# Performance work log

Hardware: AMD Instinct MI355X
Metric: run time of the kernel (lower is better)

## Reference

```python
import jax, jax.numpy as jnp
import numpy as np

B, S, C, D, P = 32, 720, 2048, 256, 96
LATENT_DIMS = [512, 128, 32]  # enc_in // 4 ** k, e_layers=3
NL = 3
ALPHA = 0.1
EPS = 1e-5


def _ln(x, g, b, eps=1e-5):
    m = jnp.mean(x, axis=-1, keepdims=True)
    v = jnp.var(x, axis=-1, keepdims=True)
    return (x - m) * jax.lax.rsqrt(v + eps) * g + b


def _cov_loss(skips, lam=ALPHA, eps=EPS):
    total = jnp.zeros((), dtype=jnp.float32)
    for x in skips[1:]:
        b, c, d = x.shape
        xr = x.reshape(b * c, d)
        xc = (xr - jnp.mean(xr, axis=0, keepdims=True)) / (jnp.std(xr, axis=0, ddof=1, keepdims=True) + eps)
        cov = xc.T @ xc / (b * c - 1) + eps * jnp.eye(d, dtype=x.dtype)
        total = total - jnp.linalg.slogdet(cov)[1] / d
    return lam * total / (len(skips) - 1)


def setup_inputs() -> dict:
    key = jax.random.key(0)
    ks = jax.random.split(key, 16)
    w = lambda k, shp: (jax.random.normal(k, shp, dtype=jnp.float32) * 0.02)
    inp = {
        'x_enc': jax.random.normal(ks[0], (B, S, C), dtype=jnp.float32),
        'x_mark_enc': jnp.zeros((B, S, 4), dtype=jnp.float32),
        'x_dec': jnp.zeros((B, P, C), dtype=jnp.float32),
        'x_mark_dec': jnp.zeros((B, P, 4), dtype=jnp.float32),
        'in_w': w(ks[1], (S, D)), 'in_b': jnp.zeros((D,), jnp.float32),
        'lq0': jax.random.normal(ks[2], (LATENT_DIMS[0], D), dtype=jnp.float32),
        'lq1': jax.random.normal(ks[3], (LATENT_DIMS[1], D), dtype=jnp.float32),
        'lq2': jax.random.normal(ks[4], (LATENT_DIMS[2], D), dtype=jnp.float32),
        'down_w': w(ks[5], (NL, 4, D, D)), 'down_b': jnp.zeros((NL, 4, D), jnp.float32),
        'down_ln': jnp.stack([jnp.ones((NL, D)), jnp.zeros((NL, D))], axis=1).astype(jnp.float32),
        'pred_w': w(ks[6], (D, D)), 'pred_b': jnp.zeros((D,), jnp.float32),
        'up_w': w(ks[7], (NL, 4, D, D)), 'up_b': jnp.zeros((NL, 4, D), jnp.float32),
        'up_ln': jnp.stack([jnp.ones((NL, D)), jnp.zeros((NL, D))], axis=1).astype(jnp.float32),
        'out_w': w(ks[8], (D, P)), 'out_b': jnp.zeros((P,), jnp.float32),
    }
    return inp


def _forward(x_enc, in_w, in_b, lqs, down_w, down_b, down_ln,
             pred_w, pred_b, up_w, up_b, up_ln, out_w, out_b):
    # instance norm over time
    means = jnp.mean(x_enc, axis=1, keepdims=True)            # [B,1,C]
    xc = x_enc - means
    stdev = jnp.sqrt(jnp.var(xc, axis=1, keepdims=True) + 1e-5)
    xn = xc / stdev
    # transpose + Linear(seq_len -> d_model): [B,C,D]
    h = jnp.einsum('bsc,sd->bcd', xn, in_w) + in_b

    scale = 1.0 / jnp.sqrt(jnp.asarray(D, dtype=h.dtype))
    skips = [h]
    x = h
    for i in range(NL):
        Wq, Wk, Wv, Wo = down_w[i]
        bq, bk, bv, bo = down_b[i]
        q = lqs[i] @ Wq + bq                                  # [Lq,D] shared over batch
        k = x @ Wk + bk                                       # [B,L,D]
        v = x @ Wv + bv
        attn = jax.nn.softmax(jnp.einsum('qd,bld->bql', q, k) * scale, axis=-1)
        o = jnp.einsum('bql,bld->bqd', attn, v) @ Wo + bo
        x = _ln(o, down_ln[i, 0], down_ln[i, 1])
        skips.append(x)

    cov = _cov_loss(skips)

    x = x @ pred_w + pred_b                                   # bottom [B,32,D]
    queries = skips[::-1][1:]                                 # [128-skip, 512-skip, base]
    for i, qin in enumerate(queries):
        Wq, Wk, Wv, Wo = up_w[i]
        bq, bk, bv, bo = up_b[i]
        q = qin @ Wq + bq                                     # [B,Lq,D]
        k = x @ Wk + bk                                       # [B,Lk,D]
        v = x @ Wv + bv
        attn = jax.nn.softmax(jnp.einsum('bqd,bld->bql', q, k) * scale, axis=-1)
        o = jnp.einsum('bql,bld->bqd', attn, v) @ Wo + bo
        x = _ln(o + qin, up_ln[i, 0], up_ln[i, 1])

    dec = (x + h) @ out_w + out_b                             # [B,C,P]
    dec = jnp.transpose(dec, (0, 2, 1))                       # [B,P,C]
    dec = dec * stdev[:, 0, :][:, None, :] + means[:, 0, :][:, None, :]
    return dec, cov


def reference(x_enc, x_mark_enc, x_dec, x_mark_dec, in_w, in_b, lq0, lq1, lq2,
              down_w, down_b, down_ln, pred_w, pred_b, up_w, up_b, up_ln, out_w, out_b):
    return _forward(x_enc, in_w, in_b, (lq0, lq1, lq2), down_w, down_b, down_ln,
                    pred_w, pred_b, up_w, up_b, up_ln, out_w, out_b)
```

## Files before the change

kernel.cpp:

```cpp
#include <hip/hip_runtime.h>
#include <hip/hip_bf16.h>
#include <math.h>

#define CDIV(a, b) (((a) + (b) - 1) / (b))
typedef long long ll;
typedef unsigned short ushort_t;

constexpr int Bn = 32;
constexpr int Sn = 720;
constexpr int SnP = 768;
constexpr int Cn = 2048;
constexpr int Dn = 256;
constexpr int Pn = 96;

typedef __attribute__((ext_vector_type(8))) short bf16x8;
typedef __attribute__((ext_vector_type(4))) float f32x4;

__device__ inline ushort_t rne1(float x) {
  unsigned u = __float_as_uint(x);
  u = (u + 0x7fffu + ((u >> 16) & 1u)) >> 16;
  return (ushort_t)u;
}
__device__ inline float b2f(ushort_t u) { return __uint_as_float(((unsigned)u) << 16); }

__device__ inline void gl_lds16(const void* g, void* l) {
  __builtin_amdgcn_global_load_lds(
      (const __attribute__((address_space(1))) void*)g,
      (__attribute__((address_space(3))) void*)l, 16, 0, 0);
}

__global__ void instnorm_stats(const float* __restrict__ x,
                               float* __restrict__ mean, float* __restrict__ stdev) {
  int c = blockIdx.x * 256 + threadIdx.x;
  int b = blockIdx.y;
  const float* p = x + (ll)b * Sn * Cn + c;
  float s = 0.f, q = 0.f;
  for (int t = 0; t < Sn; ++t) {
    float v = p[(ll)t * Cn];
    s += v; q += v * v;
  }
  float m = s / (float)Sn;
  float var = q / (float)Sn - m * m;
  var = fmaxf(var, 0.f);
  mean[b * Cn + c] = m;
  stdev[b * Cn + c] = sqrtf(var + 1e-5f);
}

__global__ void normT_kernel(const float* __restrict__ X, ushort_t* __restrict__ D,
                             const float* __restrict__ mean,
                             const float* __restrict__ stdev) {
  int b = blockIdx.z;
  __shared__ float tl[32][33];
  int t = threadIdx.x;
  int tx = t & 31, ty = t >> 5;
  int s0 = blockIdx.y * 32, c0 = blockIdx.x * 32;
#pragma unroll
  for (int e = 0; e < 4; ++e) {
    int s = s0 + ty + 8 * e;
    tl[ty + 8 * e][tx] = (s < Sn) ? X[((ll)b * Sn + s) * Cn + c0 + tx] : 0.f;
  }
  __syncthreads();
#pragma unroll
  for (int e = 0; e < 4; ++e) {
    int c = c0 + ty + 8 * e, s = s0 + tx;
    if (s < SnP) {
      float mu = mean[b * Cn + c], sd = stdev[b * Cn + c];
      float v = (s < Sn) ? (tl[tx][ty + 8 * e] - mu) / sd : 0.f;
      D[((ll)b * Cn + c) * SnP + s] = rne1(v);
    }
  }
}

__global__ void cvtT_kernel(const float* __restrict__ S, ushort_t* __restrict__ D,
                            int K, int N, int KP) {
  int z = blockIdx.z;
  S += (ll)z * K * N;
  D += (ll)z * N * KP;
  __shared__ float tl[32][33];
  int t = threadIdx.x;
  int tx = t & 31, ty = t >> 5;
  int k0 = blockIdx.y * 32, n0 = blockIdx.x * 32;
#pragma unroll
  for (int e = 0; e < 4; ++e) {
    int k = k0 + ty + 8 * e;
    tl[ty + 8 * e][tx] = (k < K && n0 + tx < N) ? S[(ll)k * N + n0 + tx] : 0.f;
  }
  __syncthreads();
#pragma unroll
  for (int e = 0; e < 4; ++e) {
    int n = n0 + ty + 8 * e, kk = k0 + tx;
    if (n < N && kk < KP) D[(ll)n * KP + kk] = rne1(tl[tx][ty + 8 * e]);
  }
}

__global__ void cvt_bf(const float* __restrict__ S, ushort_t* __restrict__ D, int n) {
  int i = blockIdx.x * 256 + threadIdx.x;
  if (i < n) D[i] = rne1(S[i]);
}

template <int MODE>
__global__ __launch_bounds__(256) void gemm_bf(
    const ushort_t* __restrict__ A, const ushort_t* __restrict__ B,
    int M, int N, int K, int lda, int ldb, ll sA, ll sB,
    const float* __restrict__ bias, float alpha,
    float* __restrict__ Cf, int ldcf, ll sCf,
    ushort_t* __restrict__ Cb, int ldcb, ll sCb) {
  int gx = gridDim.x, gy = gridDim.y;
  int nwg = gx * gy * gridDim.z;
  int wg = blockIdx.x + gx * (blockIdx.y + gy * blockIdx.z);
  if ((nwg & 7) == 0) {
    int cpx = nwg >> 3;
    wg = (wg & 7) * cpx + (wg >> 3);
  }
  int g = wg / (gx * gy);
  int rem = wg - g * (gx * gy);
  int by = rem / gx;
  int bx = rem - by * gx;

  A += (ll)g * sA;
  B += (ll)g * sB;
  if (MODE & 1) Cf += (ll)g * sCf;
  if (MODE & 14) Cb += (ll)g * sCb;
  ushort_t* Vt = nullptr;
  if (MODE & 8) Vt = (ushort_t*)Cf + (ll)g * sCf;
  __shared__ ushort_t lds_ab[2][2][128][32];
  int t = threadIdx.x;
  int m0 = by * 128, n0 = bx * 128;
  int w = t >> 6, lane = t & 63;
  int wm = (w >> 1) * 64, wn = (w & 1) * 64;
  int lrow = lane & 15, kq = lane >> 4;
  int srow = lane >> 2, skcol = (lane & 3) * 8;

  auto stage = [&](int buf, int k0) {
#pragma unroll
    for (int cc = 0; cc < 4; ++cc) {
      int c = w * 4 + cc;
      int tile = c >> 3, rb = (c & 7) * 16;
      int row = rb + srow;
      const ushort_t* src;
      if (tile == 0) {
        int gm = min(m0 + row, M - 1);
        src = &A[(ll)gm * lda + k0 + skcol];
      } else {
        int gn = min(n0 + row, N - 1);
        src = &B[(ll)gn * ldb + k0 + skcol];
      }
      gl_lds16(src, &lds_ab[buf][tile][rb][0]);
    }
  };

  f32x4 acc[4][4] = {};
  int nt = K >> 5;
  stage(0, 0);
  __syncthreads();
  int cur = 0;
  for (int it = 0; it < nt; ++it) {
    if (it + 1 < nt) stage(cur ^ 1, (it + 1) * 32);
    bf16x8 af[4], bfr[4];
#pragma unroll
    for (int i = 0; i < 4; ++i)
      af[i] = *reinterpret_cast<const bf16x8*>(&lds_ab[cur][0][wm + i * 16 + lrow][kq * 8]);
#pragma unroll
    for (int j = 0; j < 4; ++j)
      bfr[j] = *reinterpret_cast<const bf16x8*>(&lds_ab[cur][1][wn + j * 16 + lrow][kq * 8]);
#pragma unroll
    for (int i = 0; i < 4; ++i)
#pragma unroll
      for (int j = 0; j < 4; ++j)
        acc[i][j] = __builtin_amdgcn_mfma_f32_16x16x32_bf16(af[i], bfr[j],
                                                            acc[i][j], 0, 0, 0);
    __syncthreads();
    cur ^= 1;
  }
#pragma unroll
  for (int i = 0; i < 4; ++i) {
    int mb = m0 + wm + i * 16 + kq * 4;
    if (mb >= M) continue;
#pragma unroll
    for (int j = 0; j < 4; ++j) {
      int c = n0 + wn + j * 16 + lrow;
      if (c >= N) continue;
      float bv = bias ? bias[c] : 0.f;
#pragma unroll
      for (int reg = 0; reg < 4; ++reg) {
        int m = mb + reg;
        float v = acc[i][j][reg] * alpha + bv;
        if (MODE & 8) {
          if (c < 256) Cb[(ll)m * ldcb + c] = rne1(v);
          else Vt[(ll)(c - 256) * ldcf + m] = rne1(v);
        } else {
          if (MODE & 1) Cf[(ll)m * ldcf + c] = v;
          if (MODE & 2) Cb[(ll)m * ldcb + c] = rne1(v);
          if (MODE & 4) Cb[(ll)c * ldcb + m] = rne1(v);
        }
      }
    }
  }
}

__device__ inline float blk_reduce(float v, volatile float* sh, int op) {
  int lane = threadIdx.x & 63, w = threadIdx.x >> 6;
#pragma unroll
  for (int off = 32; off > 0; off >>= 1) {
    float o = __shfl_down(v, off, 64);
    v = op ? fmaxf(v, o) : (v + o);
  }
  __syncthreads();
  if (lane == 0) sh[w] = v;
  __syncthreads();
  float r = op ? fmaxf(fmaxf(sh[0], sh[1]), fmaxf(sh[2], sh[3]))
               : (sh[0] + sh[1] + sh[2] + sh[3]);
  return r;
}

template <int LL>
__global__ void softmax_bf(const ushort_t* __restrict__ S, ushort_t* __restrict__ P) {
  constexpr int NE = (LL + 255) / 256;
  __shared__ float sh[4];
  ll row = blockIdx.x;
  const ushort_t* p = S + row * (ll)LL;
  ushort_t* q = P + row * (ll)LL;
  int t = threadIdx.x;
  float e[NE];
  float mx = -INFINITY;
#pragma unroll
  for (int k = 0; k < NE; ++k) {
    int i = t + k * 256;
    if (i < LL) { e[k] = b2f(p[i]); mx = fmaxf(mx, e[k]); }
  }
  mx = blk_reduce(mx, sh, 1);
  float sum = 0.f;
#pragma unroll
  for (int k = 0; k < NE; ++k) {
    int i = t + k * 256;
    if (i < LL) { e[k] = __expf(e[k] - mx); sum += e[k]; }
  }
  sum = blk_reduce(sum, sh, 0);
  float inv = 1.f / sum;
#pragma unroll
  for (int k = 0; k < NE; ++k) {
    int i = t + k * 256;
    if (i < LL) q[i] = rne1(e[k] * inv);
  }
}

__global__ void ln_kernel(const float* __restrict__ X, const ushort_t* __restrict__ RESb,
                          float* __restrict__ Yf, ushort_t* __restrict__ Yb, int postadd,
                          const float* __restrict__ gamma, const float* __restrict__ beta) {
  __shared__ float sh[4];
  ll row = blockIdx.x;
  int t = threadIdx.x;
  float r = RESb ? b2f(RESb[row * Dn + t]) : 0.f;
  float v = X[row * Dn + t] + r;
  float m = blk_reduce(v, sh, 0) * (1.f / (float)Dn);
  float d = v - m;
  float var = blk_reduce(d * d, sh, 0) * (1.f / (float)Dn);
  float y = d * rsqrtf(var + 1e-5f) * gamma[t] + beta[t];
  if (Yf) Yf[row * Dn + t] = y;
  if (Yb) Yb[row * Dn + t] = rne1(y + (postadd ? r : 0.f));
}

__global__ void colstat_partial3(const float* __restrict__ X0,
                                 double* __restrict__ part) {
  int j = blockIdx.y;
  ll joff = (j == 0) ? 0LL : ((j == 1) ? 4194304LL : 5242880LL);
  int nrows = (j == 0) ? 16384 : ((j == 1) ? 4096 : 1024);
  const float* X = X0 + joff;
  int blk = blockIdx.x, t = threadIdx.x;
  int chunk = CDIV(nrows, 256);
  int r0 = blk * chunk, r1 = min(nrows, r0 + chunk);
  double s = 0.0, q = 0.0;
  for (int r = r0; r < r1; ++r) {
    double v = (double)X[(ll)r * Dn + t];
    s += v; q += v * v;
  }
  part[(ll)j * 131072 + blk * 512 + t] = s;
  part[(ll)j * 131072 + blk * 512 + 256 + t] = q;
}

__global__ void colstat_final3(const double* __restrict__ part,
                               float* __restrict__ cmean, float* __restrict__ cistd) {
  int j = blockIdx.x;
  int nrows = (j == 0) ? 16384 : ((j == 1) ? 4096 : 1024);
  int t = threadIdx.x;
  double s = 0.0, q = 0.0;
  for (int b = 0; b < 256; ++b) {
    s += part[(ll)j * 131072 + b * 512 + t];
    q += part[(ll)j * 131072 + b * 512 + 256 + t];
  }
  double m = s / (double)nrows;
  double var = (q - (double)nrows * m * m) / (double)(nrows - 1);
  var = fmax(var, 0.0);
  cmean[j * 256 + t] = (float)m;
  cistd[j * 256 + t] = (float)(1.0 / (sqrt(var) + 1e-5));
}

__global__ __launch_bounds__(256) void cov_gram3(const float* __restrict__ X0,
                                                 const float* __restrict__ cmean0,
                                                 const float* __restrict__ cistd0,
                                                 double* __restrict__ part) {
  int j = blockIdx.z;
  int nz = (j == 0) ? 64 : ((j == 1) ? 32 : 16);
  int z = blockIdx.y;
  if (z >= nz) return;
  int nr = (j == 0) ? 16384 : ((j == 1) ? 4096 : 1024);
  ll joff = (j == 0) ? 0LL : ((j == 1) ? 4194304LL : 5242880LL);
  const float* X = X0 + joff;
  const float* cmean = cmean0 + j * 256;
  const float* cistd = cistd0 + j * 256;
  __shared__ double Am[32][66];
  __shared__ double Bq[32][66];
  __shared__ float cmA[64], ciA[64], cmB[64], ciB[64];
  int tile = blockIdx.x;
  int mi = 0;
  while (tile >= mi + 1) { tile -= mi + 1; ++mi; }
  int nj = tile;
  int m0 = mi * 64, n0 = nj * 64;
  bool diag = (mi == nj);
  int t = threadIdx.x;
  int tx4 = (t & 15) * 4, ty4 = (t >> 4) * 4;
  if (t < 64) { cmA[t] = cmean[m0 + t]; ciA[t] = cistd[m0 + t]; }
  else if (t < 128) { cmB[t - 64] = cmean[n0 + t - 64]; ciB[t - 64] = cistd[n0 + t - 64]; }
  __syncthreads();
  int chunk = nr / nz;
  int kbeg = z * chunk, kend = kbeg + chunk;
  double acc[4][4] = {};
  const double* Bbase = diag ? &Am[0][0] : &Bq[0][0];
  for (int k0 = kbeg; k0 < kend; k0 += 32) {
#pragma unroll
    for (int e = 0; e < 8; ++e) {
      int idx = t + e * 256;
      int kk = idx >> 6, mm = idx & 63;
      float xa = X[(ll)(k0 + kk) * Dn + m0 + mm];
      Am[kk][mm] = (double)((xa - cmA[mm]) * ciA[mm]);
      if (!diag) {
        float xb = X[(ll)(k0 + kk) * Dn + n0 + mm];
        Bq[kk][mm] = (double)((xb - cmB[mm]) * ciB[mm]);
      }
    }
    __syncthreads();
#pragma unroll 4
    for (int kk = 0; kk < 32; ++kk) {
      double a[4], b[4];
#pragma unroll
      for (int q = 0; q < 4; ++q) a[q] = Am[kk][ty4 + q];
#pragma unroll
      for (int q = 0; q < 4; ++q) b[q] = Bbase[kk * 66 + tx4 + q];
#pragma unroll
      for (int i = 0; i < 4; ++i)
#pragma unroll
        for (int jj = 0; jj < 4; ++jj) acc[i][jj] += a[i] * b[jj];
    }
    __syncthreads();
  }
  ll base = ((ll)((j * 64 + z) * 10 + blockIdx.x)) * 4096;
#pragma unroll
  for (int i = 0; i < 4; ++i)
#pragma unroll
    for (int jj = 0; jj < 4; ++jj)
      part[base + (ty4 + i) * 64 + tx4 + jj] = acc[i][jj];
}

__global__ void cov_reduce3(const double* __restrict__ part, double* __restrict__ Cd0) {
  int j = blockIdx.z;
  int nz = (j == 0) ? 64 : ((j == 1) ? 32 : 16);
  int nr = (j == 0) ? 16384 : ((j == 1) ? 4096 : 1024);
  double inv = 1.0 / (double)(nr - 1);
  double* Cd = Cd0 + (ll)j * 65536;
  int tile = blockIdx.x;
  int mi = 0;
  while (tile >= mi + 1) { tile -= mi + 1; ++mi; }
  int nj = tile;
  int e = blockIdx.y * 256 + threadIdx.x;
  int rr = e >> 6, cc = e & 63;
  int m = mi * 64 + rr, n = nj * 64 + cc;
  double s0 = 0.0, s1 = 0.0, s2 = 0.0, s3 = 0.0;
  int z = 0;
  for (; z + 4 <= nz; z += 4) {
    s0 += part[((ll)((j * 64 + z + 0) * 10 + blockIdx.x)) * 4096 + e];
    s1 += part[((ll)((j * 64 + z + 1) * 10 + blockIdx.x)) * 4096 + e];
    s2 += part[((ll)((j * 64 + z + 2) * 10 + blockIdx.x)) * 4096 + e];
    s3 += part[((ll)((j * 64 + z + 3) * 10 + blockIdx.x)) * 4096 + e];
  }
  double s = ((s0 + s1) + (s2 + s3)) * inv + ((m == n) ? 1e-5 : 0.0);
  Cd[m * 256 + n] = s;
}

__global__ __launch_bounds__(256) void chol_step_a(double* __restrict__ mats, int d0) {
  double* A = mats + (ll)blockIdx.x * 65536;
  __shared__ double D[32][33];
  __shared__ double dinv[32];
  int t = threadIdx.x;
  for (int e = t; e < 1024; e += 256) {
    int i = e >> 5, j = e & 31;
    D[i][j] = (j <= i) ? A[(ll)(d0 + i) * 256 + d0 + j] : 0.0;
  }
  __syncthreads();
  if (t < 32) {
    double x[32];
#pragma unroll
    for (int j = 0; j < 32; ++j) x[j] = D[t][j];
#pragma unroll
    for (int k = 0; k < 32; ++k) {
      double piv = fmax(__shfl(x[k], k, 64), 1e-300);
      double inv = 1.0 / sqrt(piv);
      double lrk = x[k] * inv;
      x[k] = lrk;
#pragma unroll
      for (int j = k + 1; j < 32; ++j) x[j] -= lrk * __shfl(lrk, j, 64);
    }
#pragma unroll
    for (int j = 0; j < 32; ++j) D[t][j] = x[j];
    dinv[t] = 1.0 / x[t];
  }
  __syncthreads();
  int r = d0 + 32 + t;
  if (r < 256) {
    double y[32];
#pragma unroll
    for (int j = 0; j < 32; ++j) y[j] = A[(ll)r * 256 + d0 + j];
#pragma unroll
    for (int j = 0; j < 32; ++j) {
      double s = y[j];
#pragma unroll
      for (int i = 0; i < j; ++i) s -= y[i] * D[j][i];
      y[j] = s * dinv[j];
    }
#pragma unroll
    for (int j = 0; j < 32; ++j) A[(ll)r * 256 + d0 + j] = y[j];
  }
  for (int e = t; e < 1024; e += 256)
    A[(ll)(d0 + (e >> 5)) * 256 + d0 + (e & 31)] = D[e >> 5][e & 31];
}

__global__ __launch_bounds__(256) void chol_step_b(double* __restrict__ mats, int d0) {
  double* A = mats + (ll)blockIdx.y * 65536;
  int tile = blockIdx.x;
  int i = 0;
  while (tile >= i + 1) { tile -= i + 1; ++i; }
  int j = tile;
  int ri = d0 + 32 + i * 32, rj = d0 + 32 + j * 32;
  __shared__ double Li[32][33];
  __shared__ double Lj[32][33];
  int t = threadIdx.x;
  for (int e = t; e < 1024; e += 256) {
    int rr = e >> 5, kk = e & 31;
    Li[rr][kk] = A[(ll)(ri + rr) * 256 + d0 + kk];
    Lj[rr][kk] = A[(ll)(rj + rr) * 256 + d0 + kk];
  }
  __syncthreads();
  for (int e = t; e < 1024; e += 256) {
    int rr = e >> 5, cc = e & 31;
    double s = 0.0;
#pragma unroll
    for (int k = 0; k < 32; ++k) s += Li[rr][k] * Lj[cc][k];
    A[(ll)(ri + rr) * 256 + rj + cc] -= s;
  }
}

__global__ void logdet_diag(const double* __restrict__ mats, double* __restrict__ ld) {
  __shared__ double sh[4];
  const double* A = mats + (ll)blockIdx.x * 65536;
  int t = threadIdx.x;
  double lg = log(A[(ll)t * 257]);
  int lane = t & 63, w = t >> 6;
#pragma unroll
  for (int off = 32; off > 0; off >>= 1) lg += __shfl_down(lg, off, 64);
  if (lane == 0) sh[w] = lg;
  __syncthreads();
  if (t == 0) ld[blockIdx.x] = 2.0 * (sh[0] + sh[1] + sh[2] + sh[3]);
}

__global__ void cov_final(const double* __restrict__ ld, float* __restrict__ outp) {
  outp[0] = (float)(-0.1 / (3.0 * 256.0) * (ld[0] + ld[1] + ld[2]));
}

__global__ __launch_bounds__(256) void out_mfma(
    const ushort_t* __restrict__ A, const ushort_t* __restrict__ B,
    const float* __restrict__ bias, const float* __restrict__ stdev,
    const float* __restrict__ mean, float* __restrict__ out) {
  constexpr int M = Bn * Cn, N = Pn, K = Dn;
  __shared__ ushort_t lds_ab[2][128][32];
  int t = threadIdx.x;
  int nwg = gridDim.y;
  int wg = blockIdx.y;
  if ((nwg & 7) == 0) {
    int cpx = nwg >> 3;
    wg = (wg & 7) * cpx + (wg >> 3);
  }
  int m0 = wg * 128;
  int w = t >> 6, lane = t & 63;
  int wm = (w >> 1) * 64, wn = (w & 1) * 64;
  int lrow = lane & 15, kq = lane >> 4;
  int srow = lane >> 2, skcol = (lane & 3) * 8;
  f32x4 acc[4][4] = {};
  for (int k0 = 0; k0 < K; k0 += 32) {
#pragma unroll
    for (int cc = 0; cc < 4; ++cc) {
      int c = w * 4 + cc;
      int tile = c >> 3, rb = (c & 7) * 16;
      int row = rb + srow;
      const ushort_t* src;
      if (tile == 0) {
        src = &A[(ll)(m0 + row) * K + k0 + skcol];
      } else {
        int gn = min(row, N - 1);
        src = &B[(ll)gn * K + k0 + skcol];
      }
      gl_lds16(src, &lds_ab[tile][rb][0]);
    }
    __syncthreads();
    bf16x8 af[4], bfr[4];
#pragma unroll
    for (int i = 0; i < 4; ++i)
      af[i] = *reinterpret_cast<const bf16x8*>(&lds_ab[0][wm + i * 16 + lrow][kq * 8]);
#pragma unroll
    for (int j = 0; j < 4; ++j)
      bfr[j] = *reinterpret_cast<const bf16x8*>(&lds_ab[1][wn + j * 16 + lrow][kq * 8]);
#pragma unroll
    for (int i = 0; i < 4; ++i)
#pragma unroll
      for (int j = 0; j < 4; ++j)
        acc[i][j] = __builtin_amdgcn_mfma_f32_16x16x32_bf16(af[i], bfr[j],
                                                            acc[i][j], 0, 0, 0);
    __syncthreads();
  }
#pragma unroll
  for (int i = 0; i < 4; ++i) {
    int mb = m0 + wm + i * 16 + kq * 4;
#pragma unroll
    for (int j = 0; j < 4; ++j) {
      int p = wn + j * 16 + lrow;
      if (p >= N) continue;
      float bv = bias[p];
#pragma unroll
      for (int reg = 0; reg < 4; ++reg) {
        int m = mb + reg;
        int b = m >> 11, c = m & 2047;
        float v = acc[i][j][reg] + bv;
        out[((ll)(b * Pn + p)) * Cn + c] = v * stdev[m] + mean[m];
      }
    }
  }
}

extern "C" void kernel_launch(void* const* d_in, const int* in_sizes, int n_in,
                              void* d_out, int out_size, void* d_ws, size_t ws_size,
                              hipStream_t stream) {
  (void)in_sizes; (void)n_in; (void)out_size; (void)ws_size;
  const float* x_enc = (const float*)d_in[0];
  const float* in_w = (const float*)d_in[4];
  const float* in_b = (const float*)d_in[5];
  const float* lq[3] = {(const float*)d_in[6], (const float*)d_in[7],
                        (const float*)d_in[8]};
  const float* down_w = (const float*)d_in[9];
  const float* down_b = (const float*)d_in[10];
  const float* down_ln = (const float*)d_in[11];
  const float* pred_w = (const float*)d_in[12];
  const float* pred_b = (const float*)d_in[13];
  const float* up_w = (const float*)d_in[14];
  const float* up_b = (const float*)d_in[15];
  const float* up_ln = (const float*)d_in[16];
  const float* out_w = (const float*)d_in[17];
  const float* out_b = (const float*)d_in[18];
  float* out = (float*)d_out;

  float* ws = (float*)d_ws;
  size_t off = 0;
  auto alloc = [&](size_t n) {
    n = (n + 3) & ~(size_t)3;
    float* p = ws + off;
    off += n;
    return p;
  };
  float* mean = alloc((size_t)Bn * Cn);
  float* stdevv = alloc((size_t)Bn * Cn);
  float* cmean = alloc(3 * 256);
  float* cistd = alloc(3 * 256);
  double* part = (double*)alloc(3 * 256 * 512 * 2);
  double* ld = (double*)alloc(32);
  double* covd = (double*)alloc(3 * 65536 * 2);
  float* s1 = alloc((size_t)Bn * 512 * Dn);
  float* s2 = alloc((size_t)Bn * 128 * Dn);
  float* s3 = alloc((size_t)Bn * 32 * Dn);
  float* attn = alloc((size_t)Bn * 512 * 2048);
  float* sbuf = alloc((size_t)16777216);
  ushort_t* h_bf = (ushort_t*)alloc((size_t)Bn * Cn * Dn / 2);
  ushort_t* s1b = (ushort_t*)alloc((size_t)Bn * 512 * Dn / 2);
  ushort_t* s2b = (ushort_t*)alloc((size_t)Bn * 128 * Dn / 2);
  ushort_t* s3b = (ushort_t*)alloc((size_t)Bn * 32 * Dn / 2);
  ushort_t* xpb = (ushort_t*)alloc((size_t)Bn * 32 * Dn / 2);
  ushort_t* xu0b = (ushort_t*)alloc((size_t)Bn * 128 * Dn / 2);
  ushort_t* xu1b = (ushort_t*)alloc((size_t)Bn * 512 * Dn / 2);
  ushort_t* qd_b = (ushort_t*)alloc(512 * 256 / 2);
  ushort_t* lqb0 = (ushort_t*)alloc(512 * 256 / 2);
  ushort_t* lqb1 = (ushort_t*)alloc(128 * 256 / 2);
  ushort_t* lqb2 = (ushort_t*)alloc(32 * 256 / 2);
  ushort_t* in_wT = (ushort_t*)alloc(256 * SnP / 2);
  ushort_t* downT = (ushort_t*)alloc(12 * 65536 / 2);
  ushort_t* upT = (ushort_t*)alloc(12 * 65536 / 2);
  ushort_t* predT = (ushort_t*)alloc(65536 / 2);
  ushort_t* outT = (ushort_t*)alloc(96 * 256 / 2);
  ushort_t* q_bf = (ushort_t*)alloc((size_t)Bn * 2048 * Dn / 2);
  ushort_t* k_bf = (ushort_t*)alloc((size_t)Bn * 2048 * Dn / 2);
  ushort_t* vT = (ushort_t*)alloc((size_t)Bn * 2048 * Dn / 2);

  ushort_t* xnT = (ushort_t*)attn;
  ushort_t* attn_s = (ushort_t*)attn;
  ushort_t* attn_b = (ushort_t*)sbuf;
  float* o2 = sbuf;
  double* covpart = (double*)sbuf;
  const float scale = 0.0625f;
  const float* npf = nullptr;

  instnorm_stats<<<dim3(Cn / 256, Bn), 256, 0, stream>>>(x_enc, mean, stdevv);
  normT_kernel<<<dim3(Cn / 32, SnP / 32, Bn), 256, 0, stream>>>(x_enc, xnT, mean,
                                                                stdevv);
  cvtT_kernel<<<dim3(8, 8, 12), 256, 0, stream>>>(down_w, downT, 256, 256, 256);
  cvtT_kernel<<<dim3(8, 8, 12), 256, 0, stream>>>(up_w, upT, 256, 256, 256);
  cvtT_kernel<<<dim3(8, 8, 1), 256, 0, stream>>>(pred_w, predT, 256, 256, 256);
  cvtT_kernel<<<dim3(8, SnP / 32, 1), 256, 0, stream>>>(in_w, in_wT, Sn, 256, SnP);
  cvtT_kernel<<<dim3(3, 8, 1), 256, 0, stream>>>(out_w, outT, 256, Pn, 256);
  cvt_bf<<<512, 256, 0, stream>>>(lq[0], lqb0, 512 * 256);
  cvt_bf<<<128, 256, 0, stream>>>(lq[1], lqb1, 128 * 256);
  cvt_bf<<<32, 256, 0, stream>>>(lq[2], lqb2, 32 * 256);

  gemm_bf<2><<<dim3(2, 16, Bn), 256, 0, stream>>>(
      xnT, in_wT, Cn, Dn, SnP, SnP, SnP, (ll)Cn * SnP, 0, in_b, 1.f,
      nullptr, 0, 0, h_bf, Dn, (ll)Cn * Dn);

  ushort_t* lqb[3] = {lqb0, lqb1, lqb2};
  float* skf[3] = {s1, s2, s3};
  ushort_t* skb[3] = {s1b, s2b, s3b};
  int Ls[4] = {2048, 512, 128, 32};
  const ushort_t* xinb = h_bf;

  for (int i = 0; i < 3; ++i) {
    int L = Ls[i], Lq = Ls[i + 1];
    const ushort_t* WqT = downT + (size_t)(i * 4 + 0) * 65536;
    const ushort_t* WkvT = downT + (size_t)(i * 4 + 1) * 65536;
    const ushort_t* WoT = downT + (size_t)(i * 4 + 3) * 65536;
    const float* bq = down_b + (i * 4 + 0) * 256;
    const float* bkv = down_b + (i * 4 + 1) * 256;
    const float* bo = down_b + (i * 4 + 3) * 256;

    gemm_bf<2><<<dim3(2, CDIV(Lq, 128), 1), 256, 0, stream>>>(
        lqb[i], WqT, Lq, Dn, Dn, Dn, Dn, 0, 0, bq, 1.f, nullptr, 0, 0, qd_b, Dn, 0);
    gemm_bf<8><<<dim3(4, L / 128, Bn), 256, 0, stream>>>(
        xinb, WkvT, L, 512, Dn, Dn, Dn, (ll)L * Dn, 0, bkv, 1.f,
        (float*)vT, L, (ll)Dn * L, k_bf, Dn, (ll)L * Dn);
    gemm_bf<2><<<dim3(L / 128, CDIV(Lq, 128), Bn), 256, 0, stream>>>(
        qd_b, k_bf, Lq, L, Dn, Dn, Dn, 0, (ll)L * Dn, npf, scale,
        nullptr, 0, 0, attn_s, L, (ll)Lq * L);
    if (L == 2048) softmax_bf<2048><<<Bn * Lq, 256, 0, stream>>>(attn_s, attn_b);
    else if (L == 512) softmax_bf<512><<<Bn * Lq, 256, 0, stream>>>(attn_s, attn_b);
    else softmax_bf<128><<<Bn * Lq, 256, 0, stream>>>(attn_s, attn_b);
    gemm_bf<2><<<dim3(2, CDIV(Lq, 128), Bn), 256, 0, stream>>>(
        attn_b, vT, Lq, Dn, L, L, L, (ll)Lq * L, (ll)Dn * L, npf, 1.f,
        nullptr, 0, 0, q_bf, Dn, (ll)Lq * Dn);
    gemm_bf<1><<<dim3(2, CDIV(Bn * Lq, 128), 1), 256, 0, stream>>>(
        q_bf, WoT, Bn * Lq, Dn, Dn, Dn, Dn, 0, 0, bo, 1.f, o2, Dn, 0, nullptr, 0, 0);
    ln_kernel<<<Bn * Lq, 256, 0, stream>>>(o2, nullptr, skf[i], skb[i], 0,
                                           down_ln + (i * 2 + 0) * 256,
                                           down_ln + (i * 2 + 1) * 256);
    xinb = skb[i];
  }

  colstat_partial3<<<dim3(256, 3), 256, 0, stream>>>(s1, part);
  colstat_final3<<<3, 256, 0, stream>>>(part, cmean, cistd);
  cov_gram3<<<dim3(10, 64, 3), 256, 0, stream>>>(s1, cmean, cistd, covpart);
  cov_reduce3<<<dim3(10, 16, 3), 256, 0, stream>>>(covpart, covd);
  for (int kb = 0; kb < 8; ++kb) {
    chol_step_a<<<3, 256, 0, stream>>>(covd, kb * 32);
    int T = 7 - kb;
    if (T > 0)
      chol_step_b<<<dim3(T * (T + 1) / 2, 3), 256, 0, stream>>>(covd, kb * 32);
  }
  logdet_diag<<<3, 256, 0, stream>>>(covd, ld);
  cov_final<<<1, 1, 0, stream>>>(ld, out + 6291456);

  gemm_bf<2><<<dim3(2, 8, 1), 256, 0, stream>>>(
      s3b, predT, Bn * 32, Dn, Dn, Dn, Dn, 0, 0, pred_b, 1.f,
      nullptr, 0, 0, xpb, Dn, 0);

  int Lks[3] = {32, 128, 512}, Lqs[3] = {128, 512, 2048};
  const ushort_t* qinb[3] = {s2b, s1b, h_bf};
  const ushort_t* xinbs[3] = {xpb, xu0b, xu1b};
  ushort_t* xoutb[3] = {xu0b, xu1b, q_bf};
  for (int i = 0; i < 3; ++i) {
    int Lk = Lks[i], Lq = Lqs[i];
    const ushort_t* WqT = upT + (size_t)(i * 4 + 0) * 65536;
    const ushort_t* WkvT = upT + (size_t)(i * 4 + 1) * 65536;
    const ushort_t* WoT = upT + (size_t)(i * 4 + 3) * 65536;
    const float* bq = up_b + (i * 4 + 0) * 256;
    const float* bkv = up_b + (i * 4 + 1) * 256;
    const float* bo = up_b + (i * 4 + 3) * 256;

    gemm_bf<2><<<dim3(2, (Bn * Lq) / 128, 1), 256, 0, stream>>>(
        qinb[i], WqT, Bn * Lq, Dn, Dn, Dn, Dn, 0, 0, bq, 1.f,
        nullptr, 0, 0, q_bf, Dn, 0);
    gemm_bf<8><<<dim3(4, CDIV(Lk, 128), Bn), 256, 0, stream>>>(
        xinbs[i], WkvT, Lk, 512, Dn, Dn, Dn, (ll)Lk * Dn, 0, bkv, 1.f,
        (float*)vT, Lk, (ll)Dn * Lk, k_bf, Dn, (ll)Lk * Dn);
    gemm_bf<2><<<dim3(CDIV(Lk, 128), CDIV(Lq, 128), Bn), 256, 0, stream>>>(
        q_bf, k_bf, Lq, Lk, Dn, Dn, Dn, (ll)Lq * Dn, (ll)Lk * Dn, npf, scale,
        nullptr, 0, 0, attn_s, Lk, (ll)Lq * Lk);
    if (Lk == 32) softmax_bf<32><<<Bn * Lq, 256, 0, stream>>>(attn_s, attn_b);
    else if (Lk == 128) softmax_bf<128><<<Bn * Lq, 256, 0, stream>>>(attn_s, attn_b);
    else softmax_bf<512><<<Bn * Lq, 256, 0, stream>>>(attn_s, attn_b);
    gemm_bf<2><<<dim3(2, CDIV(Lq, 128), Bn), 256, 0, stream>>>(
        attn_b, vT, Lq, Dn, Lk, Lk, Lk, (ll)Lq * Lk, (ll)Dn * Lk, npf, 1.f,
        nullptr, 0, 0, q_bf, Dn, (ll)Lq * Dn);
    gemm_bf<1><<<dim3(2, (Bn * Lq) / 128, 1), 256, 0, stream>>>(
        q_bf, WoT, Bn * Lq, Dn, Dn, Dn, Dn, 0, 0, bo, 1.f, o2, Dn, 0, nullptr, 0, 0);
    ln_kernel<<<Bn * Lq, 256, 0, stream>>>(o2, qinb[i], nullptr, xoutb[i],
                                           (i == 2) ? 1 : 0,
                                           up_ln + (i * 2 + 0) * 256,
                                           up_ln + (i * 2 + 1) * 256);
  }

  out_mfma<<<dim3(1, (Bn * Cn) / 128, 1), 256, 0, stream>>>(q_bf, outT, out_b,
                                                            stdevv, mean, out);
}
```

Baseline: 1.558 ms.

## Fuse output projection GEMM with residual add and LayerNorm

Adds a gemm_ln kernel that computes the Wo projection over full 256-wide rows per 64-row block, then in its epilogue adds the bias and optional residual and applies LayerNorm. Row statistics come from shuffle and LDS reductions. This replaces the separate gemm_bf<1> plus ln_kernel pair in both the down and up paths, removing the fp32 intermediate write and read and one launch per layer. In exchange, variance is computed as E[x^2]-mean^2, which is less numerically stable, and for small M the grid has fewer blocks.

```diff
diff --git a/kernel.cpp b/kernel.cpp
--- a/kernel.cpp
+++ b/kernel.cpp
@@ -198,6 +198,121 @@
   }
 }
 
+template <int LMODE>
+__global__ __launch_bounds__(256) void gemm_ln(
+    const ushort_t* __restrict__ A, const ushort_t* __restrict__ B, int M,
+    const float* __restrict__ bias, const ushort_t* __restrict__ RESb,
+    float* __restrict__ Yf, ushort_t* __restrict__ Yb,
+    const float* __restrict__ gamma, const float* __restrict__ beta) {
+  __shared__ ushort_t lds_a[2][64][32];
+  __shared__ ushort_t lds_b[2][256][32];
+  __shared__ float lnp[4][64];
+  __shared__ float lnq[4][64];
+  int t = threadIdx.x;
+  int m0 = blockIdx.x * 64;
+  int w = t >> 6, lane = t & 63;
+  int lrow = lane & 15, kq = lane >> 4;
+  int srow = lane >> 2, skcol = (lane & 3) * 8;
+
+  auto stage = [&](int buf, int k0) {
+#pragma unroll
+    for (int cc = 0; cc < 5; ++cc) {
+      int c = w * 5 + cc;
+      if (c < 4) {
+        int row = c * 16 + srow;
+        gl_lds16(&A[(ll)(m0 + row) * 256 + k0 + skcol], &lds_a[buf][c * 16][0]);
+      } else {
+        int row = (c - 4) * 16 + srow;
+        gl_lds16(&B[(ll)row * 256 + k0 + skcol], &lds_b[buf][(c - 4) * 16][0]);
+      }
+    }
+  };
+
+  f32x4 acc[4][4] = {};
+  stage(0, 0);
+  __syncthreads();
+  int cur = 0;
+  for (int it = 0; it < 8; ++it) {
+    if (it + 1 < 8) stage(cur ^ 1, (it + 1) * 32);
+    bf16x8 af[4], bfr[4];
+#pragma unroll
+    for (int i = 0; i < 4; ++i)
+      af[i] = *reinterpret_cast<const bf16x8*>(&lds_a[cur][i * 16 + lrow][kq * 8]);
+#pragma unroll
+    for (int j = 0; j < 4; ++j)
+      bfr[j] = *reinterpret_cast<const bf16x8*>(&lds_b[cur][w * 64 + j * 16 + lrow][kq * 8]);
+#pragma unroll
+    for (int i = 0; i < 4; ++i)
+#pragma unroll
+      for (int j = 0; j < 4; ++j)
+        acc[i][j] = __builtin_amdgcn_mfma_f32_16x16x32_bf16(af[i], bfr[j],
+                                                            acc[i][j], 0, 0, 0);
+    __syncthreads();
+    cur ^= 1;
+  }
+#pragma unroll
+  for (int j = 0; j < 4; ++j) {
+    int c = w * 64 + j * 16 + lrow;
+    float bv = bias[c];
+#pragma unroll
+    for (int i = 0; i < 4; ++i)
+#pragma unroll
+      for (int reg = 0; reg < 4; ++reg) {
+        int m = m0 + i * 16 + kq * 4 + reg;
+        float v = acc[i][j][reg] + bv;
+        if (LMODE >= 1) v += b2f(RESb[(ll)m * 256 + c]);
+        acc[i][j][reg] = v;
+      }
+  }
+#pragma unroll
+  for (int i = 0; i < 4; ++i)
+#pragma unroll
+    for (int reg = 0; reg < 4; ++reg) {
+      float s1 = 0.f, s2 = 0.f;
+#pragma unroll
+      for (int j = 0; j < 4; ++j) {
+        float v = acc[i][j][reg];
+        s1 += v; s2 += v * v;
+      }
+#pragma unroll
+      for (int off = 1; off < 16; off <<= 1) {
+        s1 += __shfl_xor(s1, off, 64);
+        s2 += __shfl_xor(s2, off, 64);
+      }
+      if (lrow == 0) {
+        int rr = i * 16 + kq * 4 + reg;
+        lnp[w][rr] = s1;
+        lnq[w][rr] = s2;
+      }
+    }
+  __syncthreads();
+#pragma unroll
+  for (int i = 0; i < 4; ++i)
+#pragma unroll
+    for (int reg = 0; reg < 4; ++reg) {
+      int rr = i * 16 + kq * 4 + reg;
+      float tot = lnp[0][rr] + lnp[1][rr] + lnp[2][rr] + lnp[3][rr];
+      float tq = lnq[0][rr] + lnq[1][rr] + lnq[2][rr] + lnq[3][rr];
+      float mean = tot * (1.f / 256.f);
+      float var = fmaxf(tq * (1.f / 256.f) - mean * mean, 0.f);
+      float is = rsqrtf(var + 1e-5f);
+      int m = m0 + rr;
+#pragma unroll
+      for (int j = 0; j < 4; ++j) {
+        int c = w * 64 + j * 16 + lrow;
+        float y = (acc[i][j][reg] - mean) * is * gamma[c] + beta[c];
+        if (LMODE == 0) {
+          Yf[(ll)m * 256 + c] = y;
+          Yb[(ll)m * 256 + c] = rne1(y);
+        } else if (LMODE == 1) {
+          Yb[(ll)m * 256 + c] = rne1(y);
+        } else {
+          Yb[(ll)m * 256 + c] = rne1(y + b2f(RESb[(ll)m * 256 + c]));
+        }
+      }
+    }
+}
+
 __device__ inline float blk_reduce(float v, volatile float* sh, int op) {
   int lane = threadIdx.x & 63, w = threadIdx.x >> 6;
 #pragma unroll
@@ -242,22 +357,6 @@
     int i = t + k * 256;
     if (i < LL) q[i] = rne1(e[k] * inv);
   }
-}
-
-__global__ void ln_kernel(const float* __restrict__ X, const ushort_t* __restrict__ RESb,
-                          float* __restrict__ Yf, ushort_t* __restrict__ Yb, int postadd,
-                          const float* __restrict__ gamma, const float* __restrict__ beta) {
-  __shared__ float sh[4];
-  ll row = blockIdx.x;
-  int t = threadIdx.x;
-  float r = RESb ? b2f(RESb[row * Dn + t]) : 0.f;
-  float v = X[row * Dn + t] + r;
-  float m = blk_reduce(v, sh, 0) * (1.f / (float)Dn);
-  float d = v - m;
-  float var = blk_reduce(d * d, sh, 0) * (1.f / (float)Dn);
-  float y = d * rsqrtf(var + 1e-5f) * gamma[t] + beta[t];
-  if (Yf) Yf[row * Dn + t] = y;
-  if (Yb) Yb[row * Dn + t] = rne1(y + (postadd ? r : 0.f));
 }
 
 __global__ void colstat_partial3(const float* __restrict__ X0,
@@ -608,7 +707,6 @@
   ushort_t* xnT = (ushort_t*)attn;
   ushort_t* attn_s = (ushort_t*)attn;
   ushort_t* attn_b = (ushort_t*)sbuf;
-  float* o2 = sbuf;
   double* covpart = (double*)sbuf;
   const float scale = 0.0625f;
   const float* npf = nullptr;
@@ -658,11 +756,9 @@
     gemm_bf<2><<<dim3(2, CDIV(Lq, 128), Bn), 256, 0, stream>>>(
         attn_b, vT, Lq, Dn, L, L, L, (ll)Lq * L, (ll)Dn * L, npf, 1.f,
         nullptr, 0, 0, q_bf, Dn, (ll)Lq * Dn);
-    gemm_bf<1><<<dim3(2, CDIV(Bn * Lq, 128), 1), 256, 0, stream>>>(
-        q_bf, WoT, Bn * Lq, Dn, Dn, Dn, Dn, 0, 0, bo, 1.f, o2, Dn, 0, nullptr, 0, 0);
-    ln_kernel<<<Bn * Lq, 256, 0, stream>>>(o2, nullptr, skf[i], skb[i], 0,
-                                           down_ln + (i * 2 + 0) * 256,
-                                           down_ln + (i * 2 + 1) * 256);
+    gemm_ln<0><<<dim3((Bn * Lq) / 64), 256, 0, stream>>>(
+        q_bf, WoT, Bn * Lq, bo, nullptr, skf[i], skb[i],
+        down_ln + (i * 2 + 0) * 256, down_ln + (i * 2 + 1) * 256);
     xinb = skb[i];
   }
 
@@ -711,12 +807,15 @@
     gemm_bf<2><<<dim3(2, CDIV(Lq, 128), Bn), 256, 0, stream>>>(
         attn_b, vT, Lq, Dn, Lk, Lk, Lk, (ll)Lq * Lk, (ll)Dn * Lk, npf, 1.f,
         nullptr, 0, 0, q_bf, Dn, (ll)Lq * Dn);
-    gemm_bf<1><<<dim3(2, (Bn * Lq) / 128, 1), 256, 0, stream>>>(
-        q_bf, WoT, Bn * Lq, Dn, Dn, Dn, Dn, 0, 0, bo, 1.f, o2, Dn, 0, nullptr, 0, 0);
-    ln_kernel<<<Bn * Lq, 256, 0, stream>>>(o2, qinb[i], nullptr, xoutb[i],
-                                           (i == 2) ? 1 : 0,
-                                           up_ln + (i * 2 + 0) * 256,
-                                           up_ln + (i * 2 + 1) * 256);
+    if (i == 2) {
+      gemm_ln<2><<<dim3((Bn * Lq) / 64), 256, 0, stream>>>(
+          q_bf, WoT, Bn * Lq, bo, qinb[i], nullptr, xoutb[i],
+          up_ln + (i * 2 + 0) * 256, up_ln + (i * 2 + 1) * 256);
+    } else {
+      gemm_ln<1><<<dim3((Bn * Lq) / 64), 256, 0, stream>>>(
+          q_bf, WoT, Bn * Lq, bo, qinb[i], nullptr, xoutb[i],
+          up_ln + (i * 2 + 0) * 256, up_ln + (i * 2 + 1) * 256);
+    }
   }
 
   out_mfma<<<dim3(1, (Bn * Cn) / 128, 1), 256, 0, stream>>>(q_bf, outT, out_b,
```

Result: slower. 1.610 ms (+3.3%).
